# Kernel tuning notes

Measured on AMD Instinct MI355X. Metric: run time of the kernel, lower is better.

## Reference

```python
import jax, jax.numpy as jnp
import numpy as np

B, T = 256, 800
D_IN, H, L, V = 128, 512, 2, 128


def setup_inputs() -> dict:
    key = jax.random.key(0)
    ks = jax.random.split(key, 12)
    s = 0.1  # init scale for stability
    return {
        "W_ih0": jax.random.normal(ks[0], (4 * H, D_IN), jnp.float32) * s,
        "W_hh0": jax.random.normal(ks[1], (4 * H, H), jnp.float32) * s,
        "b_ih0": jax.random.normal(ks[2], (4 * H,), jnp.float32) * s,
        "b_hh0": jax.random.normal(ks[3], (4 * H,), jnp.float32) * s,
        "W_ih1": jax.random.normal(ks[4], (4 * H, H), jnp.float32) * s,
        "W_hh1": jax.random.normal(ks[5], (4 * H, H), jnp.float32) * s,
        "b_ih1": jax.random.normal(ks[6], (4 * H,), jnp.float32) * s,
        "b_hh1": jax.random.normal(ks[7], (4 * H,), jnp.float32) * s,
        "W_lin": jax.random.normal(ks[8], (V, H), jnp.float32) * s,
        "b_lin": jax.random.normal(ks[9], (V,), jnp.float32) * s,
        "z": jax.random.randint(ks[10], (B, T), 0, V, jnp.int32),
        "num_frames": jax.random.randint(ks[11], (B,), 100, 800, jnp.int32),
    }


def _lstm_log_prob(layers, W_lin, b_lin, z, num_frames):
    # teacher-forced inputs: step i sees one_hot(z[:, i-1]), zeros at i=0
    oh = jax.nn.one_hot(z[:, :-1], D_IN, dtype=jnp.float32)          # [B, T-1, D]
    inputs = jnp.concatenate([jnp.zeros((B, 1, D_IN), jnp.float32), oh], axis=1)
    inputs = jnp.transpose(inputs, (1, 0, 2))                         # [T, B, D]

    def step(carry, x_t):
        h, c = carry  # each [L, B, H]
        inp = x_t
        hs, cs = [], []
        for l, (Wih, Whh, bih, bhh) in enumerate(layers):
            gates = inp @ Wih.T + h[l] @ Whh.T + bih + bhh            # [B, 4H]
            i, f, g, o = jnp.split(gates, 4, axis=-1)                 # torch gate order i,f,g,o
            c_new = jax.nn.sigmoid(f) * c[l] + jax.nn.sigmoid(i) * jnp.tanh(g)
            h_new = jax.nn.sigmoid(o) * jnp.tanh(c_new)
            hs.append(h_new)
            cs.append(c_new)
            inp = h_new
        logits_t = inp @ W_lin.T + b_lin                              # [B, V]
        return (jnp.stack(hs), jnp.stack(cs)), logits_t

    h0 = jnp.zeros((L, B, H), jnp.float32)
    c0 = jnp.zeros((L, B, H), jnp.float32)
    _, logits = jax.lax.scan(step, (h0, c0), inputs)                  # [T, B, V]
    logits = jnp.transpose(logits, (1, 0, 2))                         # [B, T, V]

    logp = jax.nn.log_softmax(logits, axis=-1)
    nll = -jnp.take_along_axis(logp, z[..., None].astype(jnp.int32), axis=-1)[..., 0]  # [B, T]
    mask = (jnp.arange(T)[None, :] < num_frames[:, None]).astype(nll.dtype)
    return (nll * mask).mean(axis=-1)                                 # [B] (mean over full T, as in torch)


def reference(W_ih0, W_hh0, b_ih0, b_hh0, W_ih1, W_hh1, b_ih1, b_hh1, W_lin, b_lin, z, num_frames):
    layers = [(W_ih0, W_hh0, b_ih0, b_hh0), (W_ih1, W_hh1, b_ih1, b_hh1)]
    return _lstm_log_prob(layers, W_lin, b_lin, z, num_frames)
```

## Files before the change

kernel.cpp:

```cpp
#include <hip/hip_runtime.h>

#define TT 800

typedef __attribute__((ext_vector_type(8))) short bf16x8;
typedef __attribute__((ext_vector_type(4))) float f32x4;
typedef unsigned short u16;
typedef unsigned int u32;
typedef unsigned long long u64;

constexpr int NCW = 128, NWG = 136, RT = 32;
constexpr size_t WL0A_OFF = 0;
constexpr size_t WL0B_OFF = 2097152;
constexpr size_t WL1_OFF  = 2621440;
constexpr size_t WLIN_OFF = 6815744;
constexpr size_t H0_OFF   = 6946816;
constexpr size_t H1_OFF   = 7471104;
constexpr size_t BAR_OFF  = 7995392;
constexpr int HB = 256 * 512;
constexpr int A_ST = 520;
constexpr int G_OFF_B = 33280;
constexpr int P_OFF_B = 49792;
constexpr int LDS_BYTES = 53248;

__device__ __forceinline__ u16 f2b(float x) {
  u32 u = __float_as_uint(x);
  return (u16)((u + 0x7FFFu + ((u >> 16) & 1u)) >> 16);
}
__device__ __forceinline__ float b2f(u16 v) { return __uint_as_float(((u32)v) << 16); }
__device__ __forceinline__ float sigf(float x) { return 1.f / (1.f + __expf(-x)); }
__device__ __forceinline__ float tanh_f(float x) { float e = __expf(2.f * x); return 1.f - 2.f / (e + 1.f); }

__device__ __forceinline__ u64 ld_coh8(const u64* p) {
  return __hip_atomic_load(p, __ATOMIC_RELAXED, __HIP_MEMORY_SCOPE_AGENT);
}
__device__ __forceinline__ void st_coh8(u64* p, u64 v) {
  __hip_atomic_store(p, v, __ATOMIC_RELAXED, __HIP_MEMORY_SCOPE_AGENT);
}
__device__ __forceinline__ void fpost_l(u32* fw, u32 v) {
  *(volatile u32*)fw = v;
}
__device__ __forceinline__ void fpost_a(u32* fw, u32 v) {
  __hip_atomic_store(fw, v, __ATOMIC_RELAXED, __HIP_MEMORY_SCOPE_AGENT);
}
__device__ __forceinline__ void wave_poll(u32* Fw, int lane, u32 thr, bool lok) {
  int idx = (lane < 17) ? lane : 16;
  if (lok) {
    while (true) {
      u32 v = *(volatile u32*)(Fw + idx);
      if (__all((int)(v >= thr))) break;
      asm volatile("buffer_inv" ::: "memory");
    }
  } else {
    while (true) {
      u32 v = __hip_atomic_load(Fw + idx, __ATOMIC_RELAXED, __HIP_MEMORY_SCOPE_AGENT);
      if (__all((int)(v >= thr))) break;
      __builtin_amdgcn_s_sleep(1);
    }
  }
}
__device__ __forceinline__ void l1inv() { asm volatile("buffer_inv" ::: "memory"); }

__global__ void prep_kernel(const float* __restrict__ wih0, const float* __restrict__ whh0,
                            const float* __restrict__ wih1, const float* __restrict__ whh1,
                            const float* __restrict__ wlinf,
                            u16* __restrict__ wl0a, u16* __restrict__ wl0b,
                            u16* __restrict__ wl1, u16* __restrict__ wlin) {
  int i = blockIdx.x * 256 + threadIdx.x;
  const int NA = 2048 * 512, NB = 128 * 2048, N1 = 2048 * 1024, N2 = 128 * 512;
  if (i < NA) {
    int col = i >> 9, k = i & 511;
    wl0a[i] = f2b(whh0[col * 512 + k]);
  } else if (i < NA + NB) {
    int j = i - NA, k = j >> 11, col = j & 2047;
    wl0b[j] = f2b(wih0[col * 128 + k]);
  } else if (i < NA + NB + N1) {
    int j = i - NA - NB, col = j >> 10, k = j & 1023;
    float v = (k < 512) ? wih1[col * 512 + k] : whh1[col * 512 + (k - 512)];
    wl1[j] = f2b(v);
  } else if (i < NA + NB + N1 + N2) {
    int j = i - NA - NB - N1, col = j >> 9, k = j & 511;
    wlin[j] = f2b(wlinf[col * 512 + k]);
  }
}

__global__ __launch_bounds__(256, 1) void lstm_kernel(
    const float* __restrict__ bih0, const float* __restrict__ bhh0,
    const float* __restrict__ bih1, const float* __restrict__ bhh1,
    const float* __restrict__ blin,
    const int* __restrict__ z, const int* __restrict__ nfr,
    const u16* __restrict__ wl0a, const u16* __restrict__ wl0b,
    const u16* __restrict__ wl1, const u16* __restrict__ wlin,
    u16* __restrict__ h0buf, u16* __restrict__ h1buf,
    u32* __restrict__ bars, float* __restrict__ out) {
  extern __shared__ char smem[];
  u16* A = (u16*)smem;
  float* Gf = (float*)(smem + G_OFF_B);
  float* Pm = (float*)(smem + P_OFF_B);
  float* Ps = Pm + 256;
  float* Pt = Ps + 256;
  const int wg = blockIdx.x;
  const int w_all = wg >> 3;
  const bool isC = (w_all < 16);
  const int tile = wg & 7;
  const int w = isC ? w_all : 16;
  const int slot = isC ? w : 16;
  const int tid = threadIdx.x, lane = tid & 63, wv = tid >> 6;
  const int l15 = lane & 15, l4 = lane >> 4;
  const int row0 = tile * RT;
  u32* Fw = bars + tile * 32;
  const f32x4 VZ = {0.f, 0.f, 0.f, 0.f};
  const int rC = tid >> 3, u0C = (tid & 7) * 4;
  const int cuL = tid & 31, rgL = tid >> 5;

  float c0s[4] = {0, 0, 0, 0}, c1s[4] = {0, 0, 0, 0};
  float accN = 0.f, nflv = 0.f;
  float bias0c[2], bias1c[2], biasLc[2];
  bf16x8 bq0R[32];
  bf16x8 bq1R[64];
  bf16x8 wlR[32];

  if (isC) {
#pragma unroll
    for (int cb = 0; cb < 2; ++cb) {
      int col = wv * 512 + w * 32 + cb * 16 + l15;
      bias0c[cb] = bih0[col] + bhh0[col];
      bias1c[cb] = bih1[col] + bhh1[col];
      const u16* b0 = wl0a + (size_t)col * 512 + l4 * 8;
#pragma unroll
      for (int kb = 0; kb < 16; ++kb) bq0R[cb * 16 + kb] = *(const bf16x8*)(b0 + kb * 32);
      const u16* b1 = wl1 + (size_t)col * 1024 + l4 * 8;
#pragma unroll
      for (int kb = 0; kb < 32; ++kb) bq1R[cb * 32 + kb] = *(const bf16x8*)(b1 + kb * 32);
    }
  } else {
#pragma unroll
    for (int cb = 0; cb < 2; ++cb) {
      int colV = wv * 32 + cb * 16 + l15;
      biasLc[cb] = blin[colV];
      const u16* bL = wlin + (size_t)colV * 512 + l4 * 8;
#pragma unroll
      for (int kb = 0; kb < 16; ++kb) wlR[cb * 16 + kb] = *(const bf16x8*)(bL + kb * 32);
    }
    if (rgL == 0) nflv = (float)nfr[row0 + cuL];
  }

  u32 xcc;
  asm volatile("s_getreg_b32 %0, hwreg(HW_REG_XCC_ID)" : "=s"(xcc));
  {
    int* hls = (int*)Pm;
    if (tid == 0) {
      u32 bit = 1u << (xcc & 31u);
      __hip_atomic_fetch_or(bars + 256 + tile, bit, __ATOMIC_RELAXED, __HIP_MEMORY_SCOPE_AGENT);
      __hip_atomic_fetch_add(bars + 272, 1u, __ATOMIC_RELAXED, __HIP_MEMORY_SCOPE_AGENT);
      while (__hip_atomic_load(bars + 272, __ATOMIC_RELAXED, __HIP_MEMORY_SCOPE_AGENT) < (u32)NWG)
        __builtin_amdgcn_s_sleep(1);
      u32 m = __hip_atomic_load(bars + 256 + tile, __ATOMIC_RELAXED, __HIP_MEMORY_SCOPE_AGENT);
      hls[0] = (m == bit) ? 1 : 0;
    }
    __syncthreads();
    const_cast<volatile int&>(hls[0]);
  }
  const bool lok = (((volatile int*)Pm)[0] != 0);
  __syncthreads();

  if (isC && w == 0) {
    u64* z0 = (u64*)(h0buf + HB + row0 * 512);
    u64* z1 = (u64*)(h1buf + row0 * 512);
    u64* z2 = (u64*)(h1buf + HB + row0 * 512);
    if (lok) {
      for (int k = tid; k < 2048; k += 256) { z0[k] = 0; z1[k] = 0; z2[k] = 0; }
    } else {
      for (int k = tid; k < 2048; k += 256) { st_coh8(z0 + k, 0); st_coh8(z1 + k, 0); st_coh8(z2 + k, 0); }
    }
  }
  __syncthreads();
  if (tid == 0) { if (lok) fpost_l(Fw + slot, 1u); else fpost_a(Fw + slot, 1u); }

  auto ldA = [&](int rb, int kb) {
    return *(const bf16x8*)(A + (rb * 16 + l15) * A_ST + kb * 32 + l4 * 8);
  };

#pragma unroll 1
  for (int tau = 0; tau <= TT + 1; ++tau) {
    if (wv == 0) wave_poll(Fw, lane, (u32)(tau + 1), lok);
    __syncthreads();
    if (lok) l1inv();
    const u16* h0src = h0buf + ((tau + 1) & 1) * HB + row0 * 512;
    const u64* h1s64 = (const u64*)(h1buf + (tau & 1) * HB + row0 * 512);
    const bool l0act = isC && (tau < TT);
    const bool l1act = isC && (tau >= 1 && tau <= TT);

    if (isC) {
      if (tau <= TT) {
        u64 ta[8], tb[8];
        const u64* s64 = (const u64*)h0src;
        if (lok) {
#pragma unroll
          for (int c = 0; c < 8; ++c) {
            int li = c * 256 + tid;
            ta[c] = s64[li * 2]; tb[c] = s64[li * 2 + 1];
          }
        } else {
#pragma unroll
          for (int c = 0; c < 8; ++c) {
            int li = c * 256 + tid;
            ta[c] = ld_coh8(s64 + li * 2); tb[c] = ld_coh8(s64 + li * 2 + 1);
          }
        }
#pragma unroll
        for (int c = 0; c < 8; ++c) {
          int li = c * 256 + tid, row = li >> 6, cc = li & 63;
          u64* d = (u64*)(A + row * A_ST + cc * 8);
          d[0] = ta[c]; d[1] = tb[c];
        }
      }
      u64 ha[4], hb[4];
      if (l1act) {
        if (lok) {
#pragma unroll
          for (int c = 0; c < 4; ++c) {
            int li = c * 256 + tid;
            ha[c] = h1s64[li * 2]; hb[c] = h1s64[li * 2 + 1];
          }
        } else {
#pragma unroll
          for (int c = 0; c < 4; ++c) {
            int li = c * 256 + tid;
            ha[c] = ld_coh8(h1s64 + li * 2); hb[c] = ld_coh8(h1s64 + li * 2 + 1);
          }
        }
      }
      __syncthreads();

      f32x4 acc0[2][2] = {{VZ, VZ}, {VZ, VZ}};
      f32x4 acc1[2][2] = {{VZ, VZ}, {VZ, VZ}};
      if (l0act) {
#pragma unroll
        for (int kb = 0; kb < 16; ++kb) {
          bf16x8 a0 = ldA(0, kb), a1 = ldA(1, kb);
#pragma unroll
          for (int cb = 0; cb < 2; ++cb) {
            acc0[0][cb] = __builtin_amdgcn_mfma_f32_16x16x32_bf16(a0, bq0R[cb * 16 + kb], acc0[0][cb], 0, 0, 0);
            acc0[1][cb] = __builtin_amdgcn_mfma_f32_16x16x32_bf16(a1, bq0R[cb * 16 + kb], acc0[1][cb], 0, 0, 0);
          }
        }
      }
      if (l1act) {
#pragma unroll
        for (int kb = 0; kb < 16; ++kb) {
          bf16x8 a0 = ldA(0, kb), a1 = ldA(1, kb);
#pragma unroll
          for (int cb = 0; cb < 2; ++cb) {
            acc1[0][cb] = __builtin_amdgcn_mfma_f32_16x16x32_bf16(a0, bq1R[cb * 32 + kb], acc1[0][cb], 0, 0, 0);
            acc1[1][cb] = __builtin_amdgcn_mfma_f32_16x16x32_bf16(a1, bq1R[cb * 32 + kb], acc1[1][cb], 0, 0, 0);
          }
        }
      }
      if (l0act) {
#pragma unroll
        for (int rb = 0; rb < 2; ++rb)
#pragma unroll
          for (int cb = 0; cb < 2; ++cb)
#pragma unroll
            for (int q = 0; q < 4; ++q)
              Gf[(rb * 16 + l4 * 4 + q) * 129 + wv * 32 + cb * 16 + l15] = acc0[rb][cb][q] + bias0c[cb];
      }
      __syncthreads();

      u64 ha2[4], hb2[4];
      if (l1act) {
        if (lok) {
#pragma unroll
          for (int c = 0; c < 4; ++c) {
            int li = (c + 4) * 256 + tid;
            ha2[c] = h1s64[li * 2]; hb2[c] = h1s64[li * 2 + 1];
          }
        } else {
#pragma unroll
          for (int c = 0; c < 4; ++c) {
            int li = (c + 4) * 256 + tid;
            ha2[c] = ld_coh8(h1s64 + li * 2); hb2[c] = ld_coh8(h1s64 + li * 2 + 1);
          }
        }
      }
      if (l0act) {
        float g4[4][4];
#pragma unroll
        for (int g = 0; g < 4; ++g)
#pragma unroll
          for (int j = 0; j < 4; ++j) g4[g][j] = Gf[rC * 129 + g * 32 + u0C + j];
        if (tau >= 1) {
          int zr = z[(row0 + rC) * TT + (tau - 1)];
          const u16* gb = wl0b + (size_t)zr * 2048 + w * 32 + u0C;
#pragma unroll
          for (int g = 0; g < 4; ++g) {
            u64 v = *(const u64*)(gb + g * 512);
#pragma unroll
            for (int j = 0; j < 4; ++j) g4[g][j] += b2f((u16)(v >> (16 * j)));
          }
        }
        u64 pk = 0;
#pragma unroll
        for (int j = 0; j < 4; ++j) {
          float cn = sigf(g4[1][j]) * c0s[j] + sigf(g4[0][j]) * tanh_f(g4[2][j]);
          float hn = sigf(g4[3][j]) * tanh_f(cn);
          c0s[j] = cn;
          pk |= ((u64)f2b(hn)) << (16 * j);
        }
        u16* h0w = h0buf + (tau & 1) * HB + row0 * 512;
        u64* dst = (u64*)(h0w + rC * 512 + w * 32 + u0C);
        if (lok) *dst = pk; else st_coh8(dst, pk);
      }
      if (l1act) {
#pragma unroll
        for (int c = 0; c < 4; ++c) {
          int li = c * 256 + tid, row = li >> 6, cc = li & 63;
          u64* d = (u64*)(A + row * A_ST + cc * 8);
          d[0] = ha[c]; d[1] = hb[c];
        }
#pragma unroll
        for (int c = 0; c < 4; ++c) {
          int li = (c + 4) * 256 + tid, row = li >> 6, cc = li & 63;
          u64* d = (u64*)(A + row * A_ST + cc * 8);
          d[0] = ha2[c]; d[1] = hb2[c];
        }
      }
      __syncthreads();

      if (l1act) {
#pragma unroll
        for (int kb = 16; kb < 32; ++kb) {
          bf16x8 a0 = ldA(0, kb - 16), a1 = ldA(1, kb - 16);
#pragma unroll
          for (int cb = 0; cb < 2; ++cb) {
            acc1[0][cb] = __builtin_amdgcn_mfma_f32_16x16x32_bf16(a0, bq1R[cb * 32 + kb], acc1[0][cb], 0, 0, 0);
            acc1[1][cb] = __builtin_amdgcn_mfma_f32_16x16x32_bf16(a1, bq1R[cb * 32 + kb], acc1[1][cb], 0, 0, 0);
          }
        }
#pragma unroll
        for (int rb = 0; rb < 2; ++rb)
#pragma unroll
          for (int cb = 0; cb < 2; ++cb)
#pragma unroll
            for (int q = 0; q < 4; ++q)
              Gf[(rb * 16 + l4 * 4 + q) * 129 + wv * 32 + cb * 16 + l15] = acc1[rb][cb][q] + bias1c[cb];
      }
      __syncthreads();

      if (l1act) {
        float g4[4][4];
#pragma unroll
        for (int g = 0; g < 4; ++g)
#pragma unroll
          for (int j = 0; j < 4; ++j) g4[g][j] = Gf[rC * 129 + g * 32 + u0C + j];
        u64 pk = 0;
#pragma unroll
        for (int j = 0; j < 4; ++j) {
          float cn = sigf(g4[1][j]) * c1s[j] + sigf(g4[0][j]) * tanh_f(g4[2][j]);
          float hn = sigf(g4[3][j]) * tanh_f(cn);
          c1s[j] = cn;
          pk |= ((u64)f2b(hn)) << (16 * j);
        }
        u16* h1w = h1buf + ((tau + 1) & 1) * HB + row0 * 512;
        u64* dst = (u64*)(h1w + rC * 512 + w * 32 + u0C);
        if (lok) *dst = pk; else st_coh8(dst, pk);
      }
      __syncthreads();
      if (tid == 0) { if (lok) fpost_l(Fw + slot, (u32)(tau + 2)); else fpost_a(Fw + slot, (u32)(tau + 2)); }
    } else {
      const bool lgact = (tau >= 2);
      if (lgact) {
        u64 ta[8], tb[8];
        if (lok) {
#pragma unroll
          for (int c = 0; c < 8; ++c) {
            int li = c * 256 + tid;
            ta[c] = h1s64[li * 2]; tb[c] = h1s64[li * 2 + 1];
          }
        } else {
#pragma unroll
          for (int c = 0; c < 8; ++c) {
            int li = c * 256 + tid;
            ta[c] = ld_coh8(h1s64 + li * 2); tb[c] = ld_coh8(h1s64 + li * 2 + 1);
          }
        }
#pragma unroll
        for (int c = 0; c < 8; ++c) {
          int li = c * 256 + tid, row = li >> 6, cc = li & 63;
          u64* d = (u64*)(A + row * A_ST + cc * 8);
          d[0] = ta[c]; d[1] = tb[c];
        }
      }
      __syncthreads();
      if (tid == 0) { if (lok) fpost_l(Fw + slot, (u32)(tau + 2)); else fpost_a(Fw + slot, (u32)(tau + 2)); }
      if (lgact) {
        f32x4 accL[2][2] = {{VZ, VZ}, {VZ, VZ}};
#pragma unroll
        for (int kb = 0; kb < 16; ++kb) {
          bf16x8 a0 = ldA(0, kb), a1 = ldA(1, kb);
#pragma unroll
          for (int cb = 0; cb < 2; ++cb) {
            accL[0][cb] = __builtin_amdgcn_mfma_f32_16x16x32_bf16(a0, wlR[cb * 16 + kb], accL[0][cb], 0, 0, 0);
            accL[1][cb] = __builtin_amdgcn_mfma_f32_16x16x32_bf16(a1, wlR[cb * 16 + kb], accL[1][cb], 0, 0, 0);
          }
        }
#pragma unroll
        for (int rb = 0; rb < 2; ++rb)
#pragma unroll
          for (int cb = 0; cb < 2; ++cb)
#pragma unroll
            for (int q = 0; q < 4; ++q)
              Gf[(rb * 16 + l4 * 4 + q) * 129 + wv * 32 + cb * 16 + l15] = accL[rb][cb][q] + biasLc[cb];
      }
      __syncthreads();
      if (lgact) {
        int t2 = tau - 2;
        int r = cuL, k = rgL;
        float vloc[16], mloc = -3.4e38f;
#pragma unroll
        for (int j = 0; j < 16; ++j) {
          vloc[j] = Gf[r * 129 + k * 16 + j];
          mloc = fmaxf(mloc, vloc[j]);
        }
        Pm[r * 8 + k] = mloc;
        __syncthreads();
        float mrow = Pm[r * 8];
#pragma unroll
        for (int j = 1; j < 8; ++j) mrow = fmaxf(mrow, Pm[r * 8 + j]);
        int zr = z[(row0 + r) * TT + t2];
        float sloc = 0.f, tloc = 0.f;
#pragma unroll
        for (int j = 0; j < 16; ++j) {
          sloc += __expf(vloc[j] - mrow);
          tloc += (k * 16 + j == zr) ? vloc[j] : 0.f;
        }
        Ps[r * 8 + k] = sloc; Pt[r * 8 + k] = tloc;
        __syncthreads();
        if (k == 0) {
          float s = 0.f, tv = 0.f;
#pragma unroll
          for (int j = 0; j < 8; ++j) { s += Ps[r * 8 + j]; tv += Pt[r * 8 + j]; }
          if ((float)t2 < nflv) accN += mrow + __logf(s) - tv;
        }
      } else {
        __syncthreads(); __syncthreads();
      }
    }
  }

  if (!isC && rgL == 0) out[row0 + cuL] = accN * (1.0f / TT);
}

extern "C" void kernel_launch(void* const* d_in, const int* in_sizes, int n_in,
                              void* d_out, int out_size, void* d_ws, size_t ws_size,
                              hipStream_t stream) {
  const float* wih0 = (const float*)d_in[0];
  const float* whh0 = (const float*)d_in[1];
  const float* bih0 = (const float*)d_in[2];
  const float* bhh0 = (const float*)d_in[3];
  const float* wih1 = (const float*)d_in[4];
  const float* whh1 = (const float*)d_in[5];
  const float* bih1 = (const float*)d_in[6];
  const float* bhh1 = (const float*)d_in[7];
  const float* wlinf = (const float*)d_in[8];
  const float* blin = (const float*)d_in[9];
  const int* z = (const int*)d_in[10];
  const int* nfr = (const int*)d_in[11];
  float* out = (float*)d_out;
  char* ws = (char*)d_ws;
  u16* wl0a = (u16*)(ws + WL0A_OFF);
  u16* wl0b = (u16*)(ws + WL0B_OFF);
  u16* wl1 = (u16*)(ws + WL1_OFF);
  u16* wlin = (u16*)(ws + WLIN_OFF);
  u16* h0buf = (u16*)(ws + H0_OFF);
  u16* h1buf = (u16*)(ws + H1_OFF);
  u32* bars = (u32*)(ws + BAR_OFF);

  hipMemsetAsync(ws + BAR_OFF, 0, 2048, stream);
  const int NTOT = 2048 * 512 + 128 * 2048 + 2048 * 1024 + 128 * 512;
  prep_kernel<<<dim3((NTOT + 255) / 256), dim3(256), 0, stream>>>(
      wih0, whh0, wih1, whh1, wlinf, wl0a, wl0b, wl1, wlin);
  lstm_kernel<<<dim3(NWG), dim3(256), LDS_BYTES, stream>>>(
      bih0, bhh0, bih1, bhh1, blin, z, nfr, wl0a, wl0b, wl1, wlin, h0buf, h1buf, bars, out);
}
```

Baseline: 7.559 ms.

## Split each 32-row tile into two 16-row half-tiles with independent flag barriers

Each workgroup now processes its 32 batch rows as two independent 16-row halves (A and B), each with its own LDS staging buffer, gate buffer, cell state and flag array. Each half waits only on its own barrier, so one half's compute can overlap with other workgroups still finishing the other half, hiding inter-workgroup synchronization latency. In exchange it doubles the polls, barriers and flag posts per step and halves the MFMA work per sync, which may add overhead.

```diff
diff --git a/kernel.cpp b/kernel.cpp
--- a/kernel.cpp
+++ b/kernel.cpp
@@ -8,7 +8,7 @@
 typedef unsigned int u32;
 typedef unsigned long long u64;
 
-constexpr int NCW = 128, NWG = 136, RT = 32;
+constexpr int NWG = 136;
 constexpr size_t WL0A_OFF = 0;
 constexpr size_t WL0B_OFF = 2097152;
 constexpr size_t WL1_OFF  = 2621440;
@@ -18,8 +18,10 @@
 constexpr size_t BAR_OFF  = 7995392;
 constexpr int HB = 256 * 512;
 constexpr int A_ST = 520;
-constexpr int G_OFF_B = 33280;
-constexpr int P_OFF_B = 49792;
+constexpr int AB_OFF_B = 16640;
+constexpr int GA_OFF_B = 33280;
+constexpr int GB_OFF_B = 41536;
+constexpr int P_OFF_B  = 49792;
 constexpr int LDS_BYTES = 53248;
 
 __device__ __forceinline__ u16 f2b(float x) {
@@ -36,9 +38,10 @@
 __device__ __forceinline__ void st_coh8(u64* p, u64 v) {
   __hip_atomic_store(p, v, __ATOMIC_RELAXED, __HIP_MEMORY_SCOPE_AGENT);
 }
-__device__ __forceinline__ void fpost_l(u32* fw, u32 v) {
-  *(volatile u32*)fw = v;
-}
+__device__ __forceinline__ void st_coh4(u32* p, u32 v) {
+  __hip_atomic_store(p, v, __ATOMIC_RELAXED, __HIP_MEMORY_SCOPE_AGENT);
+}
+__device__ __forceinline__ void fpost_l(u32* fw, u32 v) { *(volatile u32*)fw = v; }
 __device__ __forceinline__ void fpost_a(u32* fw, u32 v) {
   __hip_atomic_store(fw, v, __ATOMIC_RELAXED, __HIP_MEMORY_SCOPE_AGENT);
 }
@@ -93,8 +96,10 @@
     u16* __restrict__ h0buf, u16* __restrict__ h1buf,
     u32* __restrict__ bars, float* __restrict__ out) {
   extern __shared__ char smem[];
-  u16* A = (u16*)smem;
-  float* Gf = (float*)(smem + G_OFF_B);
+  u16* AA = (u16*)smem;
+  u16* AB = (u16*)(smem + AB_OFF_B);
+  float* GfA = (float*)(smem + GA_OFF_B);
+  float* GfB = (float*)(smem + GB_OFF_B);
   float* Pm = (float*)(smem + P_OFF_B);
   float* Ps = Pm + 256;
   float* Pt = Ps + 256;
@@ -106,14 +111,17 @@
   const int slot = isC ? w : 16;
   const int tid = threadIdx.x, lane = tid & 63, wv = tid >> 6;
   const int l15 = lane & 15, l4 = lane >> 4;
-  const int row0 = tile * RT;
-  u32* Fw = bars + tile * 32;
+  const int row0 = tile * 32;
+  const int rowA = row0, rowB = row0 + 16;
+  u32* FA = bars + tile * 48;
+  u32* FB = FA + 20;
   const f32x4 VZ = {0.f, 0.f, 0.f, 0.f};
-  const int rC = tid >> 3, u0C = (tid & 7) * 4;
-  const int cuL = tid & 31, rgL = tid >> 5;
-
-  float c0s[4] = {0, 0, 0, 0}, c1s[4] = {0, 0, 0, 0};
-  float accN = 0.f, nflv = 0.f;
+  const int rC2 = tid >> 4, u0C2 = (tid & 15) * 2;
+  const int rL = tid & 15, kL = tid >> 4;
+
+  float c0A[2] = {0, 0}, c1A[2] = {0, 0};
+  float c0B[2] = {0, 0}, c1B[2] = {0, 0};
+  float accNA = 0.f, accNB = 0.f, nflA = 0.f, nflB = 0.f;
   float bias0c[2], bias1c[2], biasLc[2];
   bf16x8 bq0R[32];
   bf16x8 bq1R[64];
@@ -141,7 +149,7 @@
 #pragma unroll
       for (int kb = 0; kb < 16; ++kb) wlR[cb * 16 + kb] = *(const bf16x8*)(bL + kb * 32);
     }
-    if (rgL == 0) nflv = (float)nfr[row0 + cuL];
+    if (kL == 0) { nflA = (float)nfr[rowA + rL]; nflB = (float)nfr[rowB + rL]; }
   }
 
   u32 xcc;
@@ -150,11 +158,11 @@
     int* hls = (int*)Pm;
     if (tid == 0) {
       u32 bit = 1u << (xcc & 31u);
-      __hip_atomic_fetch_or(bars + 256 + tile, bit, __ATOMIC_RELAXED, __HIP_MEMORY_SCOPE_AGENT);
-      __hip_atomic_fetch_add(bars + 272, 1u, __ATOMIC_RELAXED, __HIP_MEMORY_SCOPE_AGENT);
-      while (__hip_atomic_load(bars + 272, __ATOMIC_RELAXED, __HIP_MEMORY_SCOPE_AGENT) < (u32)NWG)
+      __hip_atomic_fetch_or(bars + 384 + tile, bit, __ATOMIC_RELAXED, __HIP_MEMORY_SCOPE_AGENT);
+      __hip_atomic_fetch_add(bars + 392, 1u, __ATOMIC_RELAXED, __HIP_MEMORY_SCOPE_AGENT);
+      while (__hip_atomic_load(bars + 392, __ATOMIC_RELAXED, __HIP_MEMORY_SCOPE_AGENT) < (u32)NWG)
         __builtin_amdgcn_s_sleep(1);
-      u32 m = __hip_atomic_load(bars + 256 + tile, __ATOMIC_RELAXED, __HIP_MEMORY_SCOPE_AGENT);
+      u32 m = __hip_atomic_load(bars + 384 + tile, __ATOMIC_RELAXED, __HIP_MEMORY_SCOPE_AGENT);
       hls[0] = (m == bit) ? 1 : 0;
     }
     __syncthreads();
@@ -174,281 +182,473 @@
     }
   }
   __syncthreads();
-  if (tid == 0) { if (lok) fpost_l(Fw + slot, 1u); else fpost_a(Fw + slot, 1u); }
-
-  auto ldA = [&](int rb, int kb) {
-    return *(const bf16x8*)(A + (rb * 16 + l15) * A_ST + kb * 32 + l4 * 8);
+  if (tid == 0) {
+    if (lok) { fpost_l(FA + slot, 1u); fpost_l(FB + slot, 1u); }
+    else     { fpost_a(FA + slot, 1u); fpost_a(FB + slot, 1u); }
+  }
+
+  auto ldAA = [&](int kb) {
+    return *(const bf16x8*)(AA + l15 * A_ST + kb * 32 + l4 * 8);
+  };
+  auto ldAB = [&](int kb) {
+    return *(const bf16x8*)(AB + l15 * A_ST + kb * 32 + l4 * 8);
   };
 
 #pragma unroll 1
   for (int tau = 0; tau <= TT + 1; ++tau) {
-    if (wv == 0) wave_poll(Fw, lane, (u32)(tau + 1), lok);
+    const bool l0act = isC && (tau < TT);
+    const bool l1act = isC && (tau >= 1 && tau <= TT);
+    const bool lgact = (tau >= 2);
+
+    if (wv == 0) wave_poll(FA, lane, (u32)(tau + 1), lok);
     __syncthreads();
     if (lok) l1inv();
-    const u16* h0src = h0buf + ((tau + 1) & 1) * HB + row0 * 512;
-    const u64* h1s64 = (const u64*)(h1buf + (tau & 1) * HB + row0 * 512);
-    const bool l0act = isC && (tau < TT);
-    const bool l1act = isC && (tau >= 1 && tau <= TT);
-
-    if (isC) {
-      if (tau <= TT) {
-        u64 ta[8], tb[8];
-        const u64* s64 = (const u64*)h0src;
-        if (lok) {
-#pragma unroll
-          for (int c = 0; c < 8; ++c) {
-            int li = c * 256 + tid;
-            ta[c] = s64[li * 2]; tb[c] = s64[li * 2 + 1];
+    {
+      const u16* h0src = h0buf + ((tau + 1) & 1) * HB + rowA * 512;
+      const u64* h1s = (const u64*)(h1buf + (tau & 1) * HB + rowA * 512);
+      if (isC) {
+        if (tau <= TT) {
+          u64 ta[4], tb[4];
+          const u64* s64 = (const u64*)h0src;
+          if (lok) {
+#pragma unroll
+            for (int c = 0; c < 4; ++c) { int li = c * 256 + tid; ta[c] = s64[li * 2]; tb[c] = s64[li * 2 + 1]; }
+          } else {
+#pragma unroll
+            for (int c = 0; c < 4; ++c) { int li = c * 256 + tid; ta[c] = ld_coh8(s64 + li * 2); tb[c] = ld_coh8(s64 + li * 2 + 1); }
+          }
+#pragma unroll
+          for (int c = 0; c < 4; ++c) {
+            int li = c * 256 + tid, row = li >> 6, cc = li & 63;
+            u64* d = (u64*)(AA + row * A_ST + cc * 8);
+            d[0] = ta[c]; d[1] = tb[c];
+          }
+        }
+        u64 ha[2], hb[2];
+        if (l1act) {
+          if (lok) {
+#pragma unroll
+            for (int c = 0; c < 2; ++c) { int li = c * 256 + tid; ha[c] = h1s[li * 2]; hb[c] = h1s[li * 2 + 1]; }
+          } else {
+#pragma unroll
+            for (int c = 0; c < 2; ++c) { int li = c * 256 + tid; ha[c] = ld_coh8(h1s + li * 2); hb[c] = ld_coh8(h1s + li * 2 + 1); }
+          }
+        }
+        __syncthreads();
+
+        f32x4 acc0[2] = {VZ, VZ}, acc1[2] = {VZ, VZ};
+        if (l0act) {
+#pragma unroll
+          for (int kb = 0; kb < 16; ++kb) {
+            bf16x8 a0 = ldAA(kb);
+#pragma unroll
+            for (int cb = 0; cb < 2; ++cb)
+              acc0[cb] = __builtin_amdgcn_mfma_f32_16x16x32_bf16(a0, bq0R[cb * 16 + kb], acc0[cb], 0, 0, 0);
+          }
+        }
+        if (l1act) {
+#pragma unroll
+          for (int kb = 0; kb < 16; ++kb) {
+            bf16x8 a0 = ldAA(kb);
+#pragma unroll
+            for (int cb = 0; cb < 2; ++cb)
+              acc1[cb] = __builtin_amdgcn_mfma_f32_16x16x32_bf16(a0, bq1R[cb * 32 + kb], acc1[cb], 0, 0, 0);
+          }
+        }
+        if (l0act) {
+#pragma unroll
+          for (int cb = 0; cb < 2; ++cb)
+#pragma unroll
+            for (int q = 0; q < 4; ++q)
+              GfA[(l4 * 4 + q) * 129 + wv * 32 + cb * 16 + l15] = acc0[cb][q] + bias0c[cb];
+        }
+        __syncthreads();
+
+        u64 ha2[2], hb2[2];
+        if (l1act) {
+          if (lok) {
+#pragma unroll
+            for (int c = 0; c < 2; ++c) { int li = (c + 2) * 256 + tid; ha2[c] = h1s[li * 2]; hb2[c] = h1s[li * 2 + 1]; }
+          } else {
+#pragma unroll
+            for (int c = 0; c < 2; ++c) { int li = (c + 2) * 256 + tid; ha2[c] = ld_coh8(h1s + li * 2); hb2[c] = ld_coh8(h1s + li * 2 + 1); }
+          }
+        }
+        if (l0act) {
+          float g4[4][2];
+#pragma unroll
+          for (int g = 0; g < 4; ++g)
+#pragma unroll
+            for (int j = 0; j < 2; ++j) g4[g][j] = GfA[rC2 * 129 + g * 32 + u0C2 + j];
+          if (tau >= 1) {
+            int zr = z[(rowA + rC2) * TT + (tau - 1)];
+            const u16* gb = wl0b + (size_t)zr * 2048 + w * 32 + u0C2;
+#pragma unroll
+            for (int g = 0; g < 4; ++g) {
+              u32 v = *(const u32*)(gb + g * 512);
+              g4[g][0] += b2f((u16)v); g4[g][1] += b2f((u16)(v >> 16));
+            }
+          }
+          u32 pk = 0;
+#pragma unroll
+          for (int j = 0; j < 2; ++j) {
+            float cn = sigf(g4[1][j]) * c0A[j] + sigf(g4[0][j]) * tanh_f(g4[2][j]);
+            float hn = sigf(g4[3][j]) * tanh_f(cn);
+            c0A[j] = cn;
+            pk |= ((u32)f2b(hn)) << (16 * j);
+          }
+          u16* h0w = h0buf + (tau & 1) * HB + rowA * 512;
+          u32* dst = (u32*)(h0w + rC2 * 512 + w * 32 + u0C2);
+          if (lok) *dst = pk; else st_coh4(dst, pk);
+        }
+        if (l1act) {
+#pragma unroll
+          for (int c = 0; c < 2; ++c) {
+            int li = c * 256 + tid, row = li >> 6, cc = li & 63;
+            u64* d = (u64*)(AA + row * A_ST + cc * 8);
+            d[0] = ha[c]; d[1] = hb[c];
+          }
+#pragma unroll
+          for (int c = 0; c < 2; ++c) {
+            int li = (c + 2) * 256 + tid, row = li >> 6, cc = li & 63;
+            u64* d = (u64*)(AA + row * A_ST + cc * 8);
+            d[0] = ha2[c]; d[1] = hb2[c];
+          }
+        }
+        __syncthreads();
+
+        if (l1act) {
+#pragma unroll
+          for (int kb = 16; kb < 32; ++kb) {
+            bf16x8 a0 = ldAA(kb - 16);
+#pragma unroll
+            for (int cb = 0; cb < 2; ++cb)
+              acc1[cb] = __builtin_amdgcn_mfma_f32_16x16x32_bf16(a0, bq1R[cb * 32 + kb], acc1[cb], 0, 0, 0);
+          }
+#pragma unroll
+          for (int cb = 0; cb < 2; ++cb)
+#pragma unroll
+            for (int q = 0; q < 4; ++q)
+              GfA[(l4 * 4 + q) * 129 + wv * 32 + cb * 16 + l15] = acc1[cb][q] + bias1c[cb];
+        }
+        __syncthreads();
+
+        if (l1act) {
+          float g4[4][2];
+#pragma unroll
+          for (int g = 0; g < 4; ++g)
+#pragma unroll
+            for (int j = 0; j < 2; ++j) g4[g][j] = GfA[rC2 * 129 + g * 32 + u0C2 + j];
+          u32 pk = 0;
+#pragma unroll
+          for (int j = 0; j < 2; ++j) {
+            float cn = sigf(g4[1][j]) * c1A[j] + sigf(g4[0][j]) * tanh_f(g4[2][j]);
+            float hn = sigf(g4[3][j]) * tanh_f(cn);
+            c1A[j] = cn;
+            pk |= ((u32)f2b(hn)) << (16 * j);
+          }
+          u16* h1w = h1buf + ((tau + 1) & 1) * HB + rowA * 512;
+          u32* dst = (u32*)(h1w + rC2 * 512 + w * 32 + u0C2);
+          if (lok) *dst = pk; else st_coh4(dst, pk);
+        }
+        __syncthreads();
+        if (tid == 0) { if (lok) fpost_l(FA + slot, (u32)(tau + 2)); else fpost_a(FA + slot, (u32)(tau + 2)); }
+      } else {
+        if (lgact) {
+          u64 ta[4], tb[4];
+          if (lok) {
+#pragma unroll
+            for (int c = 0; c < 4; ++c) { int li = c * 256 + tid; ta[c] = h1s[li * 2]; tb[c] = h1s[li * 2 + 1]; }
+          } else {
+#pragma unroll
+            for (int c = 0; c < 4; ++c) { int li = c * 256 + tid; ta[c] = ld_coh8(h1s + li * 2); tb[c] = ld_coh8(h1s + li * 2 + 1); }
+          }
+#pragma unroll
+          for (int c = 0; c < 4; ++c) {
+            int li = c * 256 + tid, row = li >> 6, cc = li & 63;
+            u64* d = (u64*)(AA + row * A_ST + cc * 8);
+            d[0] = ta[c]; d[1] = tb[c];
+          }
+        }
+        __syncthreads();
+        if (tid == 0) { if (lok) fpost_l(FA + slot, (u32)(tau + 2)); else fpost_a(FA + slot, (u32)(tau + 2)); }
+        if (lgact) {
+          f32x4 accL[2] = {VZ, VZ};
+#pragma unroll
+          for (int kb = 0; kb < 16; ++kb) {
+            bf16x8 a0 = ldAA(kb);
+#pragma unroll
+            for (int cb = 0; cb < 2; ++cb)
+              accL[cb] = __builtin_amdgcn_mfma_f32_16x16x32_bf16(a0, wlR[cb * 16 + kb], accL[cb], 0, 0, 0);
+          }
+#pragma unroll
+          for (int cb = 0; cb < 2; ++cb)
+#pragma unroll
+            for (int q = 0; q < 4; ++q)
+              GfA[(l4 * 4 + q) * 129 + wv * 32 + cb * 16 + l15] = accL[cb][q] + biasLc[cb];
+        }
+        __syncthreads();
+        if (lgact) {
+          int t2 = tau - 2;
+          float vloc[8], mloc = -3.4e38f;
+#pragma unroll
+          for (int j = 0; j < 8; ++j) {
+            vloc[j] = GfA[rL * 129 + kL * 8 + j];
+            mloc = fmaxf(mloc, vloc[j]);
+          }
+          Pm[rL * 16 + kL] = mloc;
+          __syncthreads();
+          float mrow = Pm[rL * 16];
+#pragma unroll
+          for (int j = 1; j < 16; ++j) mrow = fmaxf(mrow, Pm[rL * 16 + j]);
+          int zr = z[(rowA + rL) * TT + t2];
+          float sloc = 0.f, tloc = 0.f;
+#pragma unroll
+          for (int j = 0; j < 8; ++j) {
+            sloc += __expf(vloc[j] - mrow);
+            tloc += (kL * 8 + j == zr) ? vloc[j] : 0.f;
+          }
+          Ps[rL * 16 + kL] = sloc; Pt[rL * 16 + kL] = tloc;
+          __syncthreads();
+          if (kL == 0) {
+            float s = 0.f, tv = 0.f;
+#pragma unroll
+            for (int j = 0; j < 16; ++j) { s += Ps[rL * 16 + j]; tv += Pt[rL * 16 + j]; }
+            if ((float)t2 < nflA) accNA += mrow + __logf(s) - tv;
           }
         } else {
-#pragma unroll
-          for (int c = 0; c < 8; ++c) {
-            int li = c * 256 + tid;
-            ta[c] = ld_coh8(s64 + li * 2); tb[c] = ld_coh8(s64 + li * 2 + 1);
-          }
-        }
-#pragma unroll
-        for (int c = 0; c < 8; ++c) {
-          int li = c * 256 + tid, row = li >> 6, cc = li & 63;
-          u64* d = (u64*)(A + row * A_ST + cc * 8);
-          d[0] = ta[c]; d[1] = tb[c];
+          __syncthreads(); __syncthreads();
         }
       }
-      u64 ha[4], hb[4];
-      if (l1act) {
-        if (lok) {
+    }
+
+    if (wv == 0) wave_poll(FB, lane, (u32)(tau + 1), lok);
+    __syncthreads();
+    if (lok) l1inv();
+    {
+      const u16* h0src = h0buf + ((tau + 1) & 1) * HB + rowB * 512;
+      const u64* h1s = (const u64*)(h1buf + (tau & 1) * HB + rowB * 512);
+      if (isC) {
+        if (tau <= TT) {
+          u64 ta[4], tb[4];
+          const u64* s64 = (const u64*)h0src;
+          if (lok) {
+#pragma unroll
+            for (int c = 0; c < 4; ++c) { int li = c * 256 + tid; ta[c] = s64[li * 2]; tb[c] = s64[li * 2 + 1]; }
+          } else {
+#pragma unroll
+            for (int c = 0; c < 4; ++c) { int li = c * 256 + tid; ta[c] = ld_coh8(s64 + li * 2); tb[c] = ld_coh8(s64 + li * 2 + 1); }
+          }
 #pragma unroll
           for (int c = 0; c < 4; ++c) {
-            int li = c * 256 + tid;
-            ha[c] = h1s64[li * 2]; hb[c] = h1s64[li * 2 + 1];
+            int li = c * 256 + tid, row = li >> 6, cc = li & 63;
+            u64* d = (u64*)(AB + row * A_ST + cc * 8);
+            d[0] = ta[c]; d[1] = tb[c];
+          }
+        }
+        u64 ha[2], hb[2];
+        if (l1act) {
+          if (lok) {
+#pragma unroll
+            for (int c = 0; c < 2; ++c) { int li = c * 256 + tid; ha[c] = h1s[li * 2]; hb[c] = h1s[li * 2 + 1]; }
+          } else {
+#pragma unroll
+            for (int c = 0; c < 2; ++c) { int li = c * 256 + tid; ha[c] = ld_coh8(h1s + li * 2); hb[c] = ld_coh8(h1s + li * 2 + 1); }
+          }
+        }
+        __syncthreads();
+
+        f32x4 acc0[2] = {VZ, VZ}, acc1[2] = {VZ, VZ};
+        if (l0act) {
+#pragma unroll
+          for (int kb = 0; kb < 16; ++kb) {
+            bf16x8 a0 = ldAB(kb);
+#pragma unroll
+            for (int cb = 0; cb < 2; ++cb)
+              acc0[cb] = __builtin_amdgcn_mfma_f32_16x16x32_bf16(a0, bq0R[cb * 16 + kb], acc0[cb], 0, 0, 0);
+          }
+        }
+        if (l1act) {
+#pragma unroll
+          for (int kb = 0; kb < 16; ++kb) {
+            bf16x8 a0 = ldAB(kb);
+#pragma unroll
+            for (int cb = 0; cb < 2; ++cb)
+              acc1[cb] = __builtin_amdgcn_mfma_f32_16x16x32_bf16(a0, bq1R[cb * 32 + kb], acc1[cb], 0, 0, 0);
+          }
+        }
+        if (l0act) {
+#pragma unroll
+          for (int cb = 0; cb < 2; ++cb)
+#pragma unroll
+            for (int q = 0; q < 4; ++q)
+              GfB[(l4 * 4 + q) * 129 + wv * 32 + cb * 16 + l15] = acc0[cb][q] + bias0c[cb];
+        }
+        __syncthreads();
+
+        u64 ha2[2], hb2[2];
+        if (l1act) {
+          if (lok) {
+#pragma unroll
+            for (int c = 0; c < 2; ++c) { int li = (c + 2) * 256 + tid; ha2[c] = h1s[li * 2]; hb2[c] = h1s[li * 2 + 1]; }
+          } else {
+#pragma unroll
+            for (int c = 0; c < 2; ++c) { int li = (c + 2) * 256 + tid; ha2[c] = ld_coh8(h1s + li * 2); hb2[c] = ld_coh8(h1s + li * 2 + 1); }
+          }
+        }
+        if (l0act) {
+          float g4[4][2];
+#pragma unroll
+          for (int g = 0; g < 4; ++g)
+#pragma unroll
+            for (int j = 0; j < 2; ++j) g4[g][j] = GfB[rC2 * 129 + g * 32 + u0C2 + j];
+          if (tau >= 1) {
+            int zr = z[(rowB + rC2) * TT + (tau - 1)];
+            const u16* gb = wl0b + (size_t)zr * 2048 + w * 32 + u0C2;
+#pragma unroll
+            for (int g = 0; g < 4; ++g) {
+              u32 v = *(const u32*)(gb + g * 512);
+              g4[g][0] += b2f((u16)v); g4[g][1] += b2f((u16)(v >> 16));
+            }
+          }
+          u32 pk = 0;
+#pragma unroll
+          for (int j = 0; j < 2; ++j) {
+            float cn = sigf(g4[1][j]) * c0B[j] + sigf(g4[0][j]) * tanh_f(g4[2][j]);
+            float hn = sigf(g4[3][j]) * tanh_f(cn);
+            c0B[j] = cn;
+            pk |= ((u32)f2b(hn)) << (16 * j);
+          }
+          u16* h0w = h0buf + (tau & 1) * HB + rowB * 512;
+          u32* dst = (u32*)(h0w + rC2 * 512 + w * 32 + u0C2);
+          if (lok) *dst = pk; else st_coh4(dst, pk);
+        }
+        if (l1act) {
+#pragma unroll
+          for (int c = 0; c < 2; ++c) {
+            int li = c * 256 + tid, row = li >> 6, cc = li & 63;
+            u64* d = (u64*)(AB + row * A_ST + cc * 8);
+            d[0] = ha[c]; d[1] = hb[c];
+          }
+#pragma unroll
+          for (int c = 0; c < 2; ++c) {
+            int li = (c + 2) * 256 + tid, row = li >> 6, cc = li & 63;
+            u64* d = (u64*)(AB + row * A_ST + cc * 8);
+            d[0] = ha2[c]; d[1] = hb2[c];
+          }
+        }
+        __syncthreads();
+
+        if (l1act) {
+#pragma unroll
+          for (int kb = 16; kb < 32; ++kb) {
+            bf16x8 a0 = ldAB(kb - 16);
+#pragma unroll
+            for (int cb = 0; cb < 2; ++cb)
+              acc1[cb] = __builtin_amdgcn_mfma_f32_16x16x32_bf16(a0, bq1R[cb * 32 + kb], acc1[cb], 0, 0, 0);
+          }
+#pragma unroll
+          for (int cb = 0; cb < 2; ++cb)
+#pragma unroll
+            for (int q = 0; q < 4; ++q)
+              GfB[(l4 * 4 + q) * 129 + wv * 32 + cb * 16 + l15] = acc1[cb][q] + bias1c[cb];
+        }
+        __syncthreads();
+
+        if (l1act) {
+          float g4[4][2];
+#pragma unroll
+          for (int g = 0; g < 4; ++g)
+#pragma unroll
+            for (int j = 0; j < 2; ++j) g4[g][j] = GfB[rC2 * 129 + g * 32 + u0C2 + j];
+          u32 pk = 0;
+#pragma unroll
+          for (int j = 0; j < 2; ++j) {
+            float cn = sigf(g4[1][j]) * c1B[j] + sigf(g4[0][j]) * tanh_f(g4[2][j]);
+            float hn = sigf(g4[3][j]) * tanh_f(cn);
+            c1B[j] = cn;
+            pk |= ((u32)f2b(hn)) << (16 * j);
+          }
+          u16* h1w = h1buf + ((tau + 1) & 1) * HB + rowB * 512;
+          u32* dst = (u32*)(h1w + rC2 * 512 + w * 32 + u0C2);
+          if (lok) *dst = pk; else st_coh4(dst, pk);
+        }
+        __syncthreads();
+        if (tid == 0) { if (lok) fpost_l(FB + slot, (u32)(tau + 2)); else fpost_a(FB + slot, (u32)(tau + 2)); }
+      } else {
+        if (lgact) {
+          u64 ta[4], tb[4];
+          if (lok) {
+#pragma unroll
+            for (int c = 0; c < 4; ++c) { int li = c * 256 + tid; ta[c] = h1s[li * 2]; tb[c] = h1s[li * 2 + 1]; }
+          } else {
+#pragma unroll
+            for (int c = 0; c < 4; ++c) { int li = c * 256 + tid; ta[c] = ld_coh8(h1s + li * 2); tb[c] = ld_coh8(h1s + li * 2 + 1); }
+          }
+#pragma unroll
+          for (int c = 0; c < 4; ++c) {
+            int li = c * 256 + tid, row = li >> 6, cc = li & 63;
+            u64* d = (u64*)(AB + row * A_ST + cc * 8);
+            d[0] = ta[c]; d[1] = tb[c];
+          }
+        }
+        __syncthreads();
+        if (tid == 0) { if (lok) fpost_l(FB + slot, (u32)(tau + 2)); else fpost_a(FB + slot, (u32)(tau + 2)); }
+        if (lgact) {
+          f32x4 accL[2] = {VZ, VZ};
+#pragma unroll
+          for (int kb = 0; kb < 16; ++kb) {
+            bf16x8 a0 = ldAB(kb);
+#pragma unroll
+            for (int cb = 0; cb < 2; ++cb)
+              accL[cb] = __builtin_amdgcn_mfma_f32_16x16x32_bf16(a0, wlR[cb * 16 + kb], accL[cb], 0, 0, 0);
+          }
+#pragma unroll
+          for (int cb = 0; cb < 2; ++cb)
+#pragma unroll
+            for (int q = 0; q < 4; ++q)
+              GfB[(l4 * 4 + q) * 129 + wv * 32 + cb * 16 + l15] = accL[cb][q] + biasLc[cb];
+        }
+        __syncthreads();
+        if (lgact) {
+          int t2 = tau - 2;
+          float vloc[8], mloc = -3.4e38f;
+#pragma unroll
+          for (int j = 0; j < 8; ++j) {
+            vloc[j] = GfB[rL * 129 + kL * 8 + j];
+            mloc = fmaxf(mloc, vloc[j]);
+          }
+          Pm[rL * 16 + kL] = mloc;
+          __syncthreads();
+          float mrow = Pm[rL * 16];
+#pragma unroll
+          for (int j = 1; j < 16; ++j) mrow = fmaxf(mrow, Pm[rL * 16 + j]);
+          int zr = z[(rowB + rL) * TT + t2];
+          float sloc = 0.f, tloc = 0.f;
+#pragma unroll
+          for (int j = 0; j < 8; ++j) {
+            sloc += __expf(vloc[j] - mrow);
+            tloc += (kL * 8 + j == zr) ? vloc[j] : 0.f;
+          }
+          Ps[rL * 16 + kL] = sloc; Pt[rL * 16 + kL] = tloc;
+          __syncthreads();
+          if (kL == 0) {
+            float s = 0.f, tv = 0.f;
+#pragma unroll
+            for (int j = 0; j < 16; ++j) { s += Ps[rL * 16 + j]; tv += Pt[rL * 16 + j]; }
+            if ((float)t2 < nflB) accNB += mrow + __logf(s) - tv;
           }
         } else {
-#pragma unroll
-          for (int c = 0; c < 4; ++c) {
-            int li = c * 256 + tid;
-            ha[c] = ld_coh8(h1s64 + li * 2); hb[c] = ld_coh8(h1s64 + li * 2 + 1);
-          }
+          __syncthreads(); __syncthreads();
         }
       }
-      __syncthreads();
-
-      f32x4 acc0[2][2] = {{VZ, VZ}, {VZ, VZ}};
-      f32x4 acc1[2][2] = {{VZ, VZ}, {VZ, VZ}};
-      if (l0act) {
-#pragma unroll
-        for (int kb = 0; kb < 16; ++kb) {
-          bf16x8 a0 = ldA(0, kb), a1 = ldA(1, kb);
-#pragma unroll
-          for (int cb = 0; cb < 2; ++cb) {
-            acc0[0][cb] = __builtin_amdgcn_mfma_f32_16x16x32_bf16(a0, bq0R[cb * 16 + kb], acc0[0][cb], 0, 0, 0);
-            acc0[1][cb] = __builtin_amdgcn_mfma_f32_16x16x32_bf16(a1, bq0R[cb * 16 + kb], acc0[1][cb], 0, 0, 0);
-          }
-        }
-      }
-      if (l1act) {
-#pragma unroll
-        for (int kb = 0; kb < 16; ++kb) {
-          bf16x8 a0 = ldA(0, kb), a1 = ldA(1, kb);
-#pragma unroll
-          for (int cb = 0; cb < 2; ++cb) {
-            acc1[0][cb] = __builtin_amdgcn_mfma_f32_16x16x32_bf16(a0, bq1R[cb * 32 + kb], acc1[0][cb], 0, 0, 0);
-            acc1[1][cb] = __builtin_amdgcn_mfma_f32_16x16x32_bf16(a1, bq1R[cb * 32 + kb], acc1[1][cb], 0, 0, 0);
-          }
-        }
-      }
-      if (l0act) {
-#pragma unroll
-        for (int rb = 0; rb < 2; ++rb)
-#pragma unroll
-          for (int cb = 0; cb < 2; ++cb)
-#pragma unroll
-            for (int q = 0; q < 4; ++q)
-              Gf[(rb * 16 + l4 * 4 + q) * 129 + wv * 32 + cb * 16 + l15] = acc0[rb][cb][q] + bias0c[cb];
-      }
-      __syncthreads();
-
-      u64 ha2[4], hb2[4];
-      if (l1act) {
-        if (lok) {
-#pragma unroll
-          for (int c = 0; c < 4; ++c) {
-            int li = (c + 4) * 256 + tid;
-            ha2[c] = h1s64[li * 2]; hb2[c] = h1s64[li * 2 + 1];
-          }
-        } else {
-#pragma unroll
-          for (int c = 0; c < 4; ++c) {
-            int li = (c + 4) * 256 + tid;
-            ha2[c] = ld_coh8(h1s64 + li * 2); hb2[c] = ld_coh8(h1s64 + li * 2 + 1);
-          }
-        }
-      }
-      if (l0act) {
-        float g4[4][4];
-#pragma unroll
-        for (int g = 0; g < 4; ++g)
-#pragma unroll
-          for (int j = 0; j < 4; ++j) g4[g][j] = Gf[rC * 129 + g * 32 + u0C + j];
-        if (tau >= 1) {
-          int zr = z[(row0 + rC) * TT + (tau - 1)];
-          const u16* gb = wl0b + (size_t)zr * 2048 + w * 32 + u0C;
-#pragma unroll
-          for (int g = 0; g < 4; ++g) {
-            u64 v = *(const u64*)(gb + g * 512);
-#pragma unroll
-            for (int j = 0; j < 4; ++j) g4[g][j] += b2f((u16)(v >> (16 * j)));
-          }
-        }
-        u64 pk = 0;
-#pragma unroll
-        for (int j = 0; j < 4; ++j) {
-          float cn = sigf(g4[1][j]) * c0s[j] + sigf(g4[0][j]) * tanh_f(g4[2][j]);
-          float hn = sigf(g4[3][j]) * tanh_f(cn);
-          c0s[j] = cn;
-          pk |= ((u64)f2b(hn)) << (16 * j);
-        }
-        u16* h0w = h0buf + (tau & 1) * HB + row0 * 512;
-        u64* dst = (u64*)(h0w + rC * 512 + w * 32 + u0C);
-        if (lok) *dst = pk; else st_coh8(dst, pk);
-      }
-      if (l1act) {
-#pragma unroll
-        for (int c = 0; c < 4; ++c) {
-          int li = c * 256 + tid, row = li >> 6, cc = li & 63;
-          u64* d = (u64*)(A + row * A_ST + cc * 8);
-          d[0] = ha[c]; d[1] = hb[c];
-        }
-#pragma unroll
-        for (int c = 0; c < 4; ++c) {
-          int li = (c + 4) * 256 + tid, row = li >> 6, cc = li & 63;
-          u64* d = (u64*)(A + row * A_ST + cc * 8);
-          d[0] = ha2[c]; d[1] = hb2[c];
-        }
-      }
-      __syncthreads();
-
-      if (l1act) {
-#pragma unroll
-        for (int kb = 16; kb < 32; ++kb) {
-          bf16x8 a0 = ldA(0, kb - 16), a1 = ldA(1, kb - 16);
-#pragma unroll
-          for (int cb = 0; cb < 2; ++cb) {
-            acc1[0][cb] = __builtin_amdgcn_mfma_f32_16x16x32_bf16(a0, bq1R[cb * 32 + kb], acc1[0][cb], 0, 0, 0);
-            acc1[1][cb] = __builtin_amdgcn_mfma_f32_16x16x32_bf16(a1, bq1R[cb * 32 + kb], acc1[1][cb], 0, 0, 0);
-          }
-        }
-#pragma unroll
-        for (int rb = 0; rb < 2; ++rb)
-#pragma unroll
-          for (int cb = 0; cb < 2; ++cb)
-#pragma unroll
-            for (int q = 0; q < 4; ++q)
-              Gf[(rb * 16 + l4 * 4 + q) * 129 + wv * 32 + cb * 16 + l15] = acc1[rb][cb][q] + bias1c[cb];
-      }
-      __syncthreads();
-
-      if (l1act) {
-        float g4[4][4];
-#pragma unroll
-        for (int g = 0; g < 4; ++g)
-#pragma unroll
-          for (int j = 0; j < 4; ++j) g4[g][j] = Gf[rC * 129 + g * 32 + u0C + j];
-        u64 pk = 0;
-#pragma unroll
-        for (int j = 0; j < 4; ++j) {
-          float cn = sigf(g4[1][j]) * c1s[j] + sigf(g4[0][j]) * tanh_f(g4[2][j]);
-          float hn = sigf(g4[3][j]) * tanh_f(cn);
-          c1s[j] = cn;
-          pk |= ((u64)f2b(hn)) << (16 * j);
-        }
-        u16* h1w = h1buf + ((tau + 1) & 1) * HB + row0 * 512;
-        u64* dst = (u64*)(h1w + rC * 512 + w * 32 + u0C);
-        if (lok) *dst = pk; else st_coh8(dst, pk);
-      }
-      __syncthreads();
-      if (tid == 0) { if (lok) fpost_l(Fw + slot, (u32)(tau + 2)); else fpost_a(Fw + slot, (u32)(tau + 2)); }
-    } else {
-      const bool lgact = (tau >= 2);
-      if (lgact) {
-        u64 ta[8], tb[8];
-        if (lok) {
-#pragma unroll
-          for (int c = 0; c < 8; ++c) {
-            int li = c * 256 + tid;
-            ta[c] = h1s64[li * 2]; tb[c] = h1s64[li * 2 + 1];
-          }
-        } else {
-#pragma unroll
-          for (int c = 0; c < 8; ++c) {
-            int li = c * 256 + tid;
-            ta[c] = ld_coh8(h1s64 + li * 2); tb[c] = ld_coh8(h1s64 + li * 2 + 1);
-          }
-        }
-#pragma unroll
-        for (int c = 0; c < 8; ++c) {
-          int li = c * 256 + tid, row = li >> 6, cc = li & 63;
-          u64* d = (u64*)(A + row * A_ST + cc * 8);
-          d[0] = ta[c]; d[1] = tb[c];
-        }
-      }
-      __syncthreads();
-      if (tid == 0) { if (lok) fpost_l(Fw + slot, (u32)(tau + 2)); else fpost_a(Fw + slot, (u32)(tau + 2)); }
-      if (lgact) {
-        f32x4 accL[2][2] = {{VZ, VZ}, {VZ, VZ}};
-#pragma unroll
-        for (int kb = 0; kb < 16; ++kb) {
-          bf16x8 a0 = ldA(0, kb), a1 = ldA(1, kb);
-#pragma unroll
-          for (int cb = 0; cb < 2; ++cb) {
-            accL[0][cb] = __builtin_amdgcn_mfma_f32_16x16x32_bf16(a0, wlR[cb * 16 + kb], accL[0][cb], 0, 0, 0);
-            accL[1][cb] = __builtin_amdgcn_mfma_f32_16x16x32_bf16(a1, wlR[cb * 16 + kb], accL[1][cb], 0, 0, 0);
-          }
-        }
-#pragma unroll
-        for (int rb = 0; rb < 2; ++rb)
-#pragma unroll
-          for (int cb = 0; cb < 2; ++cb)
-#pragma unroll
-            for (int q = 0; q < 4; ++q)
-              Gf[(rb * 16 + l4 * 4 + q) * 129 + wv * 32 + cb * 16 + l15] = accL[rb][cb][q] + biasLc[cb];
-      }
-      __syncthreads();
-      if (lgact) {
-        int t2 = tau - 2;
-        int r = cuL, k = rgL;
-        float vloc[16], mloc = -3.4e38f;
-#pragma unroll
-        for (int j = 0; j < 16; ++j) {
-          vloc[j] = Gf[r * 129 + k * 16 + j];
-          mloc = fmaxf(mloc, vloc[j]);
-        }
-        Pm[r * 8 + k] = mloc;
-        __syncthreads();
-        float mrow = Pm[r * 8];
-#pragma unroll
-        for (int j = 1; j < 8; ++j) mrow = fmaxf(mrow, Pm[r * 8 + j]);
-        int zr = z[(row0 + r) * TT + t2];
-        float sloc = 0.f, tloc = 0.f;
-#pragma unroll
-        for (int j = 0; j < 16; ++j) {
-          sloc += __expf(vloc[j] - mrow);
-          tloc += (k * 16 + j == zr) ? vloc[j] : 0.f;
-        }
-        Ps[r * 8 + k] = sloc; Pt[r * 8 + k] = tloc;
-        __syncthreads();
-        if (k == 0) {
-          float s = 0.f, tv = 0.f;
-#pragma unroll
-          for (int j = 0; j < 8; ++j) { s += Ps[r * 8 + j]; tv += Pt[r * 8 + j]; }
-          if ((float)t2 < nflv) accN += mrow + __logf(s) - tv;
-        }
-      } else {
-        __syncthreads(); __syncthreads();
-      }
-    }
-  }
-
-  if (!isC && rgL == 0) out[row0 + cuL] = accN * (1.0f / TT);
+    }
+  }
+
+  if (!isC && kL == 0) {
+    out[rowA + rL] = accNA * (1.0f / TT);
+    out[rowB + rL] = accNB * (1.0f / TT);
+  }
 }
 
 extern "C" void kernel_launch(void* const* d_in, const int* in_sizes, int n_in,
```

Result: slower. 12.03 ms (+59.1%).
